# Kernel tuning notes

Hardware: AMD Instinct MI355X
Metric: run time of the kernel (lower is better)

## Reference

```python
import jax, jax.numpy as jnp
import numpy as np

N = 8192        # number of cells/nodes
D_IN = 30       # input feature dim
P_DIM = 3       # position dim
HID = 32        # attention hidden dim
D_OUT = 30      # backbone output dim
FF = 128        # MLP hidden width
SIGMA = 0.3     # spatial decay sigma


def setup_inputs() -> dict:
    key = jax.random.key(0)
    ks = jax.random.split(key, 12)
    w = lambda k, shape: (jax.random.normal(k, shape, jnp.float32) * 0.1)
    return {
        "t": jax.random.uniform(ks[0], (1,), jnp.float32),
        "Z": jax.random.normal(ks[1], (N, D_IN + P_DIM + 1), jnp.float32),
        # SpatialAttentionLayer params (Q/K/V projections + output proj)
        "Wq": w(ks[2], (D_IN, HID)), "bq": jnp.zeros((HID,), jnp.float32),
        "Wk": w(ks[3], (D_IN, HID)), "bk": jnp.zeros((HID,), jnp.float32),
        "Wv": w(ks[4], (D_IN, HID)), "bv": jnp.zeros((HID,), jnp.float32),
        "Wo": w(ks[5], (HID, D_OUT)), "bo": jnp.zeros((D_OUT,), jnp.float32),
        # LayerNorm
        "ln_g": jnp.ones((D_OUT,), jnp.float32), "ln_b": jnp.zeros((D_OUT,), jnp.float32),
        # backbone MLP: Linear(30,128) -> SiLU -> Linear(128,30)
        "W1": w(ks[6], (D_OUT, FF)), "b1": jnp.zeros((FF,), jnp.float32),
        "W2": w(ks[7], (FF, D_OUT)), "b2": jnp.zeros((D_OUT,), jnp.float32),
        # expr_head: Linear(30,30)
        "We": w(ks[8], (D_OUT, D_OUT)), "be": jnp.zeros((D_OUT,), jnp.float32),
    }


def reference(t, Z, Wq, bq, Wk, bk, Wv, bv, Wo, bo, ln_g, ln_b, W1, b1, W2, b2, We, be):
    # Z: (N, D_IN + P_DIM + 1); last column is kinetic energy (unused in fwd)
    X = Z[:, :-1]                       # (N, 33)
    P = X[:, -P_DIM:]                   # (N, 3) positions
    F = X[:, :D_IN]                     # (N, 30) features

    # --- SpatialAttentionLayer: sigma distance-decay attention, no softmax ---
    Q = F @ Wq + bq
    K = F @ Wk + bk
    V = F @ Wv + bv
    scores = (Q @ K.T) / jnp.sqrt(jnp.float32(HID))          # (N, N)
    pn = jnp.sum(P * P, axis=1)
    d2 = jnp.maximum(pn[:, None] + pn[None, :] - 2.0 * (P @ P.T), 0.0)
    decay = jnp.exp(-d2 / (2.0 * SIGMA * SIGMA))              # spatial decay kernel
    A = jax.nn.sigmoid(scores) * decay                        # no-softmax attention
    A = A / (jnp.sum(A, axis=1, keepdims=True) + 1e-8)        # row-normalized message passing
    H = (A @ V) @ Wo + bo                                     # (N, D_OUT)

    # --- LayerNorm(output_dim) ---
    mu = jnp.mean(H, axis=-1, keepdims=True)
    var = jnp.mean((H - mu) ** 2, axis=-1, keepdims=True)
    Hn = (H - mu) * jax.lax.rsqrt(var + 1e-5) * ln_g + ln_b

    # --- Linear(30,128) -> SiLU -> Linear(128,30) ---
    H2 = jax.nn.silu(Hn @ W1 + b1) @ W2 + b2

    # --- expr_head ---
    feature_velo = H2 @ We + be                               # (N, 30)

    # static_pos=True -> zero position velocities (velocity_head bypassed)
    pos_velo = jnp.zeros_like(P)                              # (N, 3)

    # kinetic energy term
    ke = 0.5 * jnp.mean(feature_velo ** 2, axis=1) + 0.5 * jnp.mean(pos_velo ** 2, axis=1)
    return jnp.concatenate([feature_velo, pos_velo, ke[:, None]], axis=1)  # (N, 34)
```

## Files before the change

### kernel.cpp

```cpp
#include <hip/hip_runtime.h>
#include <hip/hip_bf16.h>

#define N      8192
#define D_IN   30
#define HID    32
#define D_OUT  30
#define FFD    128
#define ZC     34
#define JGC    16

typedef __attribute__((ext_vector_type(8))) short short8;
typedef __attribute__((ext_vector_type(16))) float f32x16;

static __device__ __forceinline__ ushort f2bf(float x) {
    uint32_t u = __float_as_uint(x);
    uint32_t r = (u + 0x7fffu + ((u >> 16) & 1u)) >> 16;
    return (ushort)r;
}
static __device__ __forceinline__ float bf2f(ushort u) {
    return __uint_as_float(((uint32_t)u) << 16);
}
static __device__ __forceinline__ float rdlane(float v, int l) {
    return __uint_as_float(__builtin_amdgcn_readlane(__float_as_uint(v), l));
}

__global__ __launch_bounds__(256) void dv_qkv_kernel(
    const float* __restrict__ Z,
    const float* __restrict__ Wq, const float* __restrict__ bq,
    const float* __restrict__ Wk, const float* __restrict__ bk,
    const float* __restrict__ Wv, const float* __restrict__ bv,
    const float* __restrict__ Wo,
    const float* __restrict__ W2, const float* __restrict__ We,
    const float* __restrict__ b2, const float* __restrict__ be,
    ushort* __restrict__ Qb, ushort* __restrict__ Kb,
    ushort* __restrict__ VWot, ushort* __restrict__ KA,
    ushort* __restrict__ QB, float* __restrict__ W2e, float* __restrict__ b2e)
{
    __shared__ ushort sv[8][33];
    const int t = blockIdx.x * 256 + threadIdx.x;
    const int i = t >> 5;
    const int h = t & 31;
    const float* z = Z + (size_t)i * ZC;

    float q = bq[h], k = bk[h], v = bv[h];
#pragma unroll
    for (int d = 0; d < D_IN; ++d) {
        float zf = z[d];
        q = fmaf(zf, Wq[d * HID + h], q);
        k = fmaf(zf, Wk[d * HID + h], k);
        v = fmaf(zf, Wv[d * HID + h], v);
    }
    const float QS = 0.17677669529663687f * 1.4426950408889634f;
    Qb[(size_t)i * HID + h] = f2bf(q * QS);
    Kb[(size_t)i * HID + h] = f2bf(k);
    sv[threadIdx.x >> 5][h] = f2bf(v);

    if (h == 0) {
        float p0 = z[D_IN], p1 = z[D_IN + 1], p2 = z[D_IN + 2];
        const float C2 = 1.4426950408889634f / 0.18f;
        const float SC = sqrtf(2.0f * C2);
        float px = p0 * SC, py = p1 * SC, pz = p2 * SC;
        float w  = -C2 * (p0 * p0 + p1 * p1 + p2 * p2);
        ushort phx = f2bf(px), phy = f2bf(py), phz = f2bf(pz);
        ushort plx = f2bf(px - bf2f(phx));
        ushort ply = f2bf(py - bf2f(phy));
        ushort plz = f2bf(pz - bf2f(phz));
        ushort wh  = f2bf(w);
        ushort wl  = f2bf(w - bf2f(wh));
        ushort nhx = phx ^ 0x8000, nhy = phy ^ 0x8000, nhz = phz ^ 0x8000;
        ushort nlx = plx ^ 0x8000, nly = ply ^ 0x8000, nlz = plz ^ 0x8000;
        ushort nwh = wh ^ 0x8000,  nwl = wl ^ 0x8000;
        const ushort one = 0x3F80, none = 0xBF80;
        ushort ka0[8] = {nwh, nwl, none, none, nhx, nhy, nhz, nhx};
        ushort ka1[8] = {nhy, nhz, nlx, nly, nlz, nlx, nly, nlz};
        ushort qb0[8] = {one, one, wh, wl, phx, phy, phz, plx};
        ushort qb1[8] = {ply, plz, phx, phy, phz, plx, ply, plz};
        *(uint4*)&KA[(size_t)i * 8]       = *(uint4*)ka0;
        *(uint4*)&KA[((size_t)N + i) * 8] = *(uint4*)ka1;
        *(uint4*)&QB[(size_t)i * 8]       = *(uint4*)qb0;
        *(uint4*)&QB[((size_t)N + i) * 8] = *(uint4*)qb1;
    }

    if (blockIdx.x < 15) {
        int idx = blockIdx.x * 256 + threadIdx.x;
        int f = idx / 30, o = idx - f * 30;
        float acc = 0.f;
#pragma unroll
        for (int d = 0; d < D_OUT; ++d)
            acc = fmaf(W2[f * D_OUT + d], We[d * D_OUT + o], acc);
        W2e[idx] = acc;
        if (idx < D_OUT) {
            float a2 = be[idx];
#pragma unroll
            for (int d = 0; d < D_OUT; ++d)
                a2 = fmaf(b2[d], We[d * D_OUT + idx], a2);
            b2e[idx] = a2;
        }
    }

    __syncthreads();
    const int io = threadIdx.x >> 5, c = threadIdx.x & 31;
    const int ii = blockIdx.x * 8 + io;
    float val;
    if (c < 30) {
        float acc = 0.f;
#pragma unroll
        for (int hh = 0; hh < HID; ++hh)
            acc = fmaf(bf2f(sv[io][hh]), Wo[hh * D_OUT + c], acc);
        val = acc;
    } else {
        val = (c == 31) ? 1.0f : 0.f;
    }
    VWot[(size_t)c * N + ii] = f2bf(val);
}

__global__ __launch_bounds__(256, 2) void dv_attn_kernel(
    const ushort* __restrict__ Qb, const ushort* __restrict__ Kb,
    const ushort* __restrict__ VWot, const ushort* __restrict__ KA,
    const ushort* __restrict__ QB, float* __restrict__ partial, int nch)
{
    __shared__ ushort lK[128 * 32];
    __shared__ ushort lV[32 * 128];
    __shared__ ushort lKA[2][128 * 8];

    const int tid  = threadIdx.x;
    const int lane = tid & 63;
    const int wv   = tid >> 6;
    const int h2   = lane >> 5;
    const int l31  = lane & 31;
    const int rb   = blockIdx.x & 63;
    const int jg   = blockIdx.x >> 6;
    const int i0w  = rb * 128 + wv * 32;

    const ushort* qp = Qb + (size_t)(i0w + l31) * HID + h2 * 8;
    const short8 qf0 = *(const short8*)qp;
    const short8 qf1 = *(const short8*)(qp + 16);
    const short8 qaug = *(const short8*)&QB[((size_t)h2 * N + i0w + l31) * 8];

    f32x16 zacc, oacc;
#pragma unroll
    for (int r = 0; r < 16; ++r) { zacc[r] = 0.f; oacc[r] = 0.f; }

    const int cA0 = (h2 + (l31 >> 1)) & 3;
    const int cA1 = (cA0 + 2) & 3;

    const int kjr0 = tid >> 2,          kcc0 = tid & 3;
    const int kjr1 = (tid + 256) >> 2,  kcc1 = (tid + 256) & 3;
    const int kc20 = (kcc0 + (kjr0 >> 1)) & 3;
    const int kc21 = (kcc1 + (kjr1 >> 1)) & 3;
    const int vhh[4] = { tid >> 5, (tid + 256) >> 5, (tid + 512) >> 5, (tid + 768) >> 5 };
    const int vcx = tid & 31;
    const int ahalf = tid >> 7, ajj = tid & 127;

    uint4 kreg[2];
    uint2 vreg[4];
    uint4 kareg;

    {
        const int j0 = (jg * nch) << 7;
        kreg[0] = *(const uint4*)&Kb[(size_t)(j0 + kjr0) * HID + kcc0 * 8];
        kreg[1] = *(const uint4*)&Kb[(size_t)(j0 + kjr1) * HID + kcc1 * 8];
#pragma unroll
        for (int r2 = 0; r2 < 4; ++r2)
            vreg[r2] = *(const uint2*)&VWot[(size_t)vhh[r2] * N + j0 + vcx * 4];
        kareg = *(const uint4*)&KA[((size_t)ahalf * N + j0 + ajj) * 8];
    }

    for (int ch = 0; ch < nch; ++ch) {
        __syncthreads();
        *(uint4*)&lK[kjr0 * 32 + kc20 * 8] = kreg[0];
        *(uint4*)&lK[kjr1 * 32 + kc21 * 8] = kreg[1];
#pragma unroll
        for (int r2 = 0; r2 < 4; ++r2)
            *(uint2*)&lV[vhh[r2] * 128 + (vcx ^ vhh[r2]) * 4] = vreg[r2];
        *(uint4*)&lKA[ahalf][ajj * 8] = kareg;
        __syncthreads();

        if (ch + 1 < nch) {
            const int j1 = (jg * nch + ch + 1) << 7;
            kreg[0] = *(const uint4*)&Kb[(size_t)(j1 + kjr0) * HID + kcc0 * 8];
            kreg[1] = *(const uint4*)&Kb[(size_t)(j1 + kjr1) * HID + kcc1 * 8];
#pragma unroll
            for (int r2 = 0; r2 < 4; ++r2)
                vreg[r2] = *(const uint2*)&VWot[(size_t)vhh[r2] * N + j1 + vcx * 4];
            kareg = *(const uint4*)&KA[((size_t)ahalf * N + j1 + ajj) * 8];
        }

#pragma unroll
        for (int t32 = 0; t32 < 4; ++t32) {
            const ushort* krow = &lK[(t32 * 32 + l31) * 32];
            short8 kf0 = *(const short8*)&krow[cA0 * 8];
            short8 kf1 = *(const short8*)&krow[cA1 * 8];
            f32x16 s = __builtin_amdgcn_mfma_f32_32x32x16_bf16(kf0, qf0, zacc, 0, 0, 0);
            s = __builtin_amdgcn_mfma_f32_32x32x16_bf16(kf1, qf1, s, 0, 0, 0);

            short8 kaug = *(const short8*)&lKA[h2][(t32 * 32 + l31) * 8];
            f32x16 gA = __builtin_amdgcn_mfma_f32_32x32x16_bf16(kaug, qaug, zacc, 0, 0, 0);

            uint32_t pk[8];
#pragma unroll
            for (int p = 0; p < 8; ++p) {
                float eg0 = __builtin_amdgcn_exp2f(-gA[2 * p]);
                float es0 = __builtin_amdgcn_exp2f(-s[2 * p]);
                float a0  = eg0 * __builtin_amdgcn_rcpf(1.0f + es0);
                float eg1 = __builtin_amdgcn_exp2f(-gA[2 * p + 1]);
                float es1 = __builtin_amdgcn_exp2f(-s[2 * p + 1]);
                float a1  = eg1 * __builtin_amdgcn_rcpf(1.0f + es1);
                asm("v_cvt_pk_bf16_f32 %0, %1, %2" : "=v"(pk[p]) : "v"(a0), "v"(a1));
            }
            union BV { uint32_t u[4]; short8 v; };
            BV fa, fb;
            fa.u[0] = pk[0]; fa.u[1] = pk[1]; fa.u[2] = pk[2]; fa.u[3] = pk[3];
            fb.u[0] = pk[4]; fb.u[1] = pk[5]; fb.u[2] = pk[6]; fb.u[3] = pk[7];

            const ushort* vrow = &lV[l31 * 128];
            const int cb = t32 * 8 + h2;
            BV b0, b1;
            *(uint2*)&b0.u[0] = *(const uint2*)&vrow[((cb    ) ^ l31) * 4];
            *(uint2*)&b0.u[2] = *(const uint2*)&vrow[((cb + 2) ^ l31) * 4];
            *(uint2*)&b1.u[0] = *(const uint2*)&vrow[((cb + 4) ^ l31) * 4];
            *(uint2*)&b1.u[2] = *(const uint2*)&vrow[((cb + 6) ^ l31) * 4];

            oacc = __builtin_amdgcn_mfma_f32_32x32x16_bf16(fa.v, b0.v, oacc, 0, 0, 0);
            oacc = __builtin_amdgcn_mfma_f32_32x32x16_bf16(fb.v, b1.v, oacc, 0, 0, 0);
        }
    }

#pragma unroll
    for (int r = 0; r < 16; ++r) {
        int ir = (r & 3) + 8 * (r >> 2) + 4 * h2 + i0w;
        partial[(size_t)ir * (JGC * 32) + jg * 32 + l31] = oacc[r];
    }
}

__global__ __launch_bounds__(256) void dv_epilogue_kernel(
    const float* __restrict__ partial,
    const float* __restrict__ bo,
    const float* __restrict__ ln_g, const float* __restrict__ ln_b,
    const float* __restrict__ W1, const float* __restrict__ b1,
    const float* __restrict__ W2e, const float* __restrict__ b2e,
    float* __restrict__ out)
{
    __shared__ float shf[4][FFD];

    const int tid  = threadIdx.x;
    const int wv   = tid >> 6;
    const int lane = tid & 63;
    const int row  = blockIdx.x * 4 + wv;
    const int c    = lane & 31;
    const bool a30 = c < 30;
    const int  c30 = a30 ? c : 0;

    float s8 = 0.f;
    {
        const float* pp = partial + (size_t)row * (JGC * 32) + lane;
#pragma unroll
        for (int q = 0; q < 8; ++q) s8 += pp[q * 64];
    }
    float sv = s8 + __shfl_xor(s8, 32, 64);

    float rsum = __shfl(sv, 31, 32);
    float inv  = __builtin_amdgcn_rcpf(rsum + 1e-8f);
    float Hl   = a30 ? fmaf(sv, inv, bo[c30]) : 0.f;

    float x = Hl;
#pragma unroll
    for (int m = 1; m < 32; m <<= 1) x += __shfl_xor(x, m, 32);
    float mu = x * (1.0f / D_OUT);
    float d  = a30 ? (Hl - mu) : 0.f;
    float v2 = d * d;
#pragma unroll
    for (int m = 1; m < 32; m <<= 1) v2 += __shfl_xor(v2, m, 32);
    float rs = rsqrtf(v2 * (1.0f / D_OUT) + 1e-5f);
    float Hn = fmaf(d * rs, ln_g[c30], ln_b[c30]);

    float acc0 = b1[lane], acc1 = b1[lane + 64];
#pragma unroll
    for (int o = 0; o < D_OUT; ++o) {
        float ho = rdlane(Hn, o);
        acc0 = fmaf(ho, W1[o * FFD + lane], acc0);
        acc1 = fmaf(ho, W1[o * FFD + lane + 64], acc1);
    }
    const float L2E = 1.4426950408889634f;
    shf[wv][lane] =
        acc0 * __builtin_amdgcn_rcpf(1.0f + __builtin_amdgcn_exp2f(-acc0 * L2E));
    shf[wv][lane + 64] =
        acc1 * __builtin_amdgcn_rcpf(1.0f + __builtin_amdgcn_exp2f(-acc1 * L2E));

    const int half = lane >> 5;
    float acc = 0.f;
    {
        const float* hbase = &shf[wv][half * 64];
#pragma unroll
        for (int k = 0; k < 16; ++k) {
            float4 hv = *(const float4*)&hbase[k * 4];
            const int f0 = half * 64 + k * 4;
            acc = fmaf(hv.x, W2e[(f0    ) * D_OUT + c30], acc);
            acc = fmaf(hv.y, W2e[(f0 + 1) * D_OUT + c30], acc);
            acc = fmaf(hv.z, W2e[(f0 + 2) * D_OUT + c30], acc);
            acc = fmaf(hv.w, W2e[(f0 + 3) * D_OUT + c30], acc);
        }
    }
    float val = acc + __shfl_xor(acc, 32, 64) + b2e[c30];

    if (lane < 32 && a30)
        out[(size_t)row * ZC + c] = val;

    float kep = a30 ? val * val : 0.f;
#pragma unroll
    for (int m = 1; m < 32; m <<= 1) kep += __shfl_xor(kep, m, 32);
    if (lane == 0) {
        float* op = out + (size_t)row * ZC;
        op[30] = 0.f; op[31] = 0.f; op[32] = 0.f;
        op[33] = kep * (0.5f / D_OUT);
    }
}

extern "C" void kernel_launch(void* const* d_in, const int* in_sizes, int n_in,
                              void* d_out, int out_size, void* d_ws, size_t ws_size,
                              hipStream_t stream)
{
    const float* Z  = (const float*)d_in[1];
    const float* Wq = (const float*)d_in[2];
    const float* bq = (const float*)d_in[3];
    const float* Wk = (const float*)d_in[4];
    const float* bk = (const float*)d_in[5];
    const float* Wv = (const float*)d_in[6];
    const float* bv = (const float*)d_in[7];
    const float* Wo = (const float*)d_in[8];
    const float* bo = (const float*)d_in[9];
    const float* lg = (const float*)d_in[10];
    const float* lb = (const float*)d_in[11];
    const float* W1 = (const float*)d_in[12];
    const float* b1 = (const float*)d_in[13];
    const float* W2 = (const float*)d_in[14];
    const float* b2 = (const float*)d_in[15];
    const float* We = (const float*)d_in[16];
    const float* be = (const float*)d_in[17];
    float* out = (float*)d_out;

    ushort* Qb   = (ushort*)d_ws;
    ushort* Kb   = Qb + (size_t)N * HID;
    ushort* VWot = Kb + (size_t)N * HID;
    ushort* KA   = VWot + (size_t)N * HID;
    ushort* QB   = KA + (size_t)N * 16;
    float*  W2e  = (float*)(QB + (size_t)N * 16);
    float*  b2e  = W2e + FFD * D_OUT;
    float*  partial = b2e + 32;

    int nch = N / (JGC * 128);

    hipLaunchKernelGGL(dv_qkv_kernel, dim3((N * HID) / 256), dim3(256), 0, stream,
                       Z, Wq, bq, Wk, bk, Wv, bv, Wo, W2, We, b2, be,
                       Qb, Kb, VWot, KA, QB, W2e, b2e);
    hipLaunchKernelGGL(dv_attn_kernel, dim3(64 * JGC), dim3(256), 0, stream,
                       Qb, Kb, VWot, KA, QB, partial, nch);
    hipLaunchKernelGGL(dv_epilogue_kernel, dim3(N / 4), dim3(256), 0, stream,
                       partial, bo, lg, lb, W1, b1, W2e, b2e, out);
}
```

Baseline: 58.44 us.

## Morton-sort points and cull far key chunks via AABB distance test

Adds a spatial sort: points are binned into a 16^3 Morton grid with histogram, scan and scatter kernels. Q/K/V are built in sorted order, and an AABB kernel computes per-128-point chunk bounds. The attention kernel skips any key chunk whose box distance to the query block makes the Gaussian decay below about 2^-24. The intent is to avoid most of the N^2 attention work. In exchange it adds five extra launches plus a memset and atomics, introduces a tiny approximation error, and may unbalance work across blocks.

```diff
diff --git a/kernel.cpp b/kernel.cpp
--- a/kernel.cpp
+++ b/kernel.cpp
@@ -8,6 +8,9 @@
 #define FFD    128
 #define ZC     34
 #define JGC    16
+#define NCH    4
+#define NCHUNK 64
+#define DCUT2  48.0f
 
 typedef __attribute__((ext_vector_type(8))) short short8;
 typedef __attribute__((ext_vector_type(16))) float f32x16;
@@ -24,8 +27,57 @@
     return __uint_as_float(__builtin_amdgcn_readlane(__float_as_uint(v), l));
 }
 
+__global__ __launch_bounds__(256) void dv_hist_kernel(
+    const float* __restrict__ Z, int* __restrict__ key, int* __restrict__ hist)
+{
+    const int i = blockIdx.x * 256 + threadIdx.x;
+    const float* z = Z + (size_t)i * ZC;
+    float x = z[D_IN], y = z[D_IN + 1], w = z[D_IN + 2];
+    int qx = (int)((x + 3.f) * (16.f / 6.f)); qx = qx < 0 ? 0 : (qx > 15 ? 15 : qx);
+    int qy = (int)((y + 3.f) * (16.f / 6.f)); qy = qy < 0 ? 0 : (qy > 15 ? 15 : qy);
+    int qz = (int)((w + 3.f) * (16.f / 6.f)); qz = qz < 0 ? 0 : (qz > 15 ? 15 : qz);
+    int k = 0;
+#pragma unroll
+    for (int b = 0; b < 4; ++b) {
+        k |= ((qx >> b) & 1) << (3 * b + 2);
+        k |= ((qy >> b) & 1) << (3 * b + 1);
+        k |= ((qz >> b) & 1) << (3 * b);
+    }
+    key[i] = k;
+    atomicAdd(&hist[k], 1);
+}
+
+__global__ __launch_bounds__(256) void dv_scan_kernel(
+    const int* __restrict__ hist, int* __restrict__ offs)
+{
+    __shared__ int ls[256];
+    const int t = threadIdx.x;
+    int loc[16], s = 0;
+#pragma unroll
+    for (int k = 0; k < 16; ++k) { loc[k] = hist[t * 16 + k]; s += loc[k]; }
+    ls[t] = s;
+    __syncthreads();
+    for (int d = 1; d < 256; d <<= 1) {
+        int v = (t >= d) ? ls[t - d] : 0;
+        __syncthreads();
+        ls[t] += v;
+        __syncthreads();
+    }
+    int excl = ls[t] - s;
+#pragma unroll
+    for (int k = 0; k < 16; ++k) { offs[t * 16 + k] = excl; excl += loc[k]; }
+}
+
+__global__ __launch_bounds__(256) void dv_scatter_kernel(
+    const int* __restrict__ key, int* __restrict__ offs, int* __restrict__ perm)
+{
+    const int i = blockIdx.x * 256 + threadIdx.x;
+    int dst = atomicAdd(&offs[key[i]], 1);
+    perm[dst] = i;
+}
+
 __global__ __launch_bounds__(256) void dv_qkv_kernel(
-    const float* __restrict__ Z,
+    const float* __restrict__ Z, const int* __restrict__ perm,
     const float* __restrict__ Wq, const float* __restrict__ bq,
     const float* __restrict__ Wk, const float* __restrict__ bk,
     const float* __restrict__ Wv, const float* __restrict__ bv,
@@ -34,13 +86,15 @@
     const float* __restrict__ b2, const float* __restrict__ be,
     ushort* __restrict__ Qb, ushort* __restrict__ Kb,
     ushort* __restrict__ VWot, ushort* __restrict__ KA,
-    ushort* __restrict__ QB, float* __restrict__ W2e, float* __restrict__ b2e)
+    ushort* __restrict__ QB, float4* __restrict__ pos_s,
+    float* __restrict__ W2e, float* __restrict__ b2e)
 {
     __shared__ ushort sv[8][33];
     const int t = blockIdx.x * 256 + threadIdx.x;
     const int i = t >> 5;
     const int h = t & 31;
-    const float* z = Z + (size_t)i * ZC;
+    const int orig = perm[i];
+    const float* z = Z + (size_t)orig * ZC;
 
     float q = bq[h], k = bk[h], v = bv[h];
 #pragma unroll
@@ -61,6 +115,7 @@
         const float SC = sqrtf(2.0f * C2);
         float px = p0 * SC, py = p1 * SC, pz = p2 * SC;
         float w  = -C2 * (p0 * p0 + p1 * p1 + p2 * p2);
+        pos_s[i] = make_float4(px, py, pz, 0.f);
         ushort phx = f2bf(px), phy = f2bf(py), phz = f2bf(pz);
         ushort plx = f2bf(px - bf2f(phx));
         ushort ply = f2bf(py - bf2f(phy));
@@ -114,10 +169,41 @@
     VWot[(size_t)c * N + ii] = f2bf(val);
 }
 
+__global__ __launch_bounds__(128) void dv_aabb_kernel(
+    const float4* __restrict__ pos_s, float4* __restrict__ aabb)
+{
+    const int cid = blockIdx.x, t = threadIdx.x;
+    float4 p = pos_s[cid * 128 + t];
+    float mnx = p.x, mny = p.y, mnz = p.z;
+    float mxx = p.x, mxy = p.y, mxz = p.z;
+#pragma unroll
+    for (int m = 1; m < 64; m <<= 1) {
+        mnx = fminf(mnx, __shfl_xor(mnx, m, 64));
+        mny = fminf(mny, __shfl_xor(mny, m, 64));
+        mnz = fminf(mnz, __shfl_xor(mnz, m, 64));
+        mxx = fmaxf(mxx, __shfl_xor(mxx, m, 64));
+        mxy = fmaxf(mxy, __shfl_xor(mxy, m, 64));
+        mxz = fmaxf(mxz, __shfl_xor(mxz, m, 64));
+    }
+    __shared__ float4 smn[2], smx[2];
+    if ((t & 63) == 0) {
+        smn[t >> 6] = make_float4(mnx, mny, mnz, 0.f);
+        smx[t >> 6] = make_float4(mxx, mxy, mxz, 0.f);
+    }
+    __syncthreads();
+    if (t == 0) {
+        float4 a = smn[0], b = smn[1];
+        aabb[cid * 2] = make_float4(fminf(a.x, b.x), fminf(a.y, b.y), fminf(a.z, b.z), 0.f);
+        a = smx[0]; b = smx[1];
+        aabb[cid * 2 + 1] = make_float4(fmaxf(a.x, b.x), fmaxf(a.y, b.y), fmaxf(a.z, b.z), 0.f);
+    }
+}
+
 __global__ __launch_bounds__(256, 2) void dv_attn_kernel(
     const ushort* __restrict__ Qb, const ushort* __restrict__ Kb,
     const ushort* __restrict__ VWot, const ushort* __restrict__ KA,
-    const ushort* __restrict__ QB, float* __restrict__ partial, int nch)
+    const ushort* __restrict__ QB, const float4* __restrict__ aabb,
+    float* __restrict__ partial)
 {
     __shared__ ushort lK[128 * 32];
     __shared__ ushort lV[32 * 128];
@@ -144,6 +230,21 @@
     const int cA0 = (h2 + (l31 >> 1)) & 3;
     const int cA1 = (cA0 + 2) & 3;
 
+    uint32_t mask = 0;
+    {
+        float4 amin = aabb[2 * rb], amax = aabb[2 * rb + 1];
+#pragma unroll
+        for (int c = 0; c < NCH; ++c) {
+            int cid = jg * NCH + c;
+            float4 bmin = aabb[2 * cid], bmax = aabb[2 * cid + 1];
+            float dx = fmaxf(0.f, fmaxf(amin.x - bmax.x, bmin.x - amax.x));
+            float dy = fmaxf(0.f, fmaxf(amin.y - bmax.y, bmin.y - amax.y));
+            float dz = fmaxf(0.f, fmaxf(amin.z - bmax.z, bmin.z - amax.z));
+            float d2 = fmaf(dx, dx, fmaf(dy, dy, dz * dz));
+            if (d2 > DCUT2) mask |= (1u << c);
+        }
+    }
+
     const int kjr0 = tid >> 2,          kcc0 = tid & 3;
     const int kjr1 = (tid + 256) >> 2,  kcc1 = (tid + 256) & 3;
     const int kc20 = (kcc0 + (kjr0 >> 1)) & 3;
@@ -156,17 +257,26 @@
     uint2 vreg[4];
     uint4 kareg;
 
-    {
-        const int j0 = (jg * nch) << 7;
+    auto LOADC = [&](int c) {
+        const int j0 = (jg * NCH + c) << 7;
         kreg[0] = *(const uint4*)&Kb[(size_t)(j0 + kjr0) * HID + kcc0 * 8];
         kreg[1] = *(const uint4*)&Kb[(size_t)(j0 + kjr1) * HID + kcc1 * 8];
 #pragma unroll
         for (int r2 = 0; r2 < 4; ++r2)
             vreg[r2] = *(const uint2*)&VWot[(size_t)vhh[r2] * N + j0 + vcx * 4];
         kareg = *(const uint4*)&KA[((size_t)ahalf * N + j0 + ajj) * 8];
-    }
-
-    for (int ch = 0; ch < nch; ++ch) {
+    };
+
+    int cur = -1;
+    for (int c = 0; c < NCH; ++c)
+        if (!(mask & (1u << c))) { cur = c; break; }
+    if (cur >= 0) LOADC(cur);
+
+    while (cur >= 0) {
+        int nxt = -1;
+        for (int c = cur + 1; c < NCH; ++c)
+            if (!(mask & (1u << c))) { nxt = c; break; }
+
         __syncthreads();
         *(uint4*)&lK[kjr0 * 32 + kc20 * 8] = kreg[0];
         *(uint4*)&lK[kjr1 * 32 + kc21 * 8] = kreg[1];
@@ -176,15 +286,7 @@
         *(uint4*)&lKA[ahalf][ajj * 8] = kareg;
         __syncthreads();
 
-        if (ch + 1 < nch) {
-            const int j1 = (jg * nch + ch + 1) << 7;
-            kreg[0] = *(const uint4*)&Kb[(size_t)(j1 + kjr0) * HID + kcc0 * 8];
-            kreg[1] = *(const uint4*)&Kb[(size_t)(j1 + kjr1) * HID + kcc1 * 8];
-#pragma unroll
-            for (int r2 = 0; r2 < 4; ++r2)
-                vreg[r2] = *(const uint2*)&VWot[(size_t)vhh[r2] * N + j1 + vcx * 4];
-            kareg = *(const uint4*)&KA[((size_t)ahalf * N + j1 + ajj) * 8];
-        }
+        if (nxt >= 0) LOADC(nxt);
 
 #pragma unroll
         for (int t32 = 0; t32 < 4; ++t32) {
@@ -224,6 +326,7 @@
             oacc = __builtin_amdgcn_mfma_f32_32x32x16_bf16(fa.v, b0.v, oacc, 0, 0, 0);
             oacc = __builtin_amdgcn_mfma_f32_32x32x16_bf16(fb.v, b1.v, oacc, 0, 0, 0);
         }
+        cur = nxt;
     }
 
 #pragma unroll
@@ -234,7 +337,7 @@
 }
 
 __global__ __launch_bounds__(256) void dv_epilogue_kernel(
-    const float* __restrict__ partial,
+    const float* __restrict__ partial, const int* __restrict__ perm,
     const float* __restrict__ bo,
     const float* __restrict__ ln_g, const float* __restrict__ ln_b,
     const float* __restrict__ W1, const float* __restrict__ b1,
@@ -247,6 +350,7 @@
     const int wv   = tid >> 6;
     const int lane = tid & 63;
     const int row  = blockIdx.x * 4 + wv;
+    const int orow = perm[row];
     const int c    = lane & 31;
     const bool a30 = c < 30;
     const int  c30 = a30 ? c : 0;
@@ -304,13 +408,13 @@
     float val = acc + __shfl_xor(acc, 32, 64) + b2e[c30];
 
     if (lane < 32 && a30)
-        out[(size_t)row * ZC + c] = val;
+        out[(size_t)orow * ZC + c] = val;
 
     float kep = a30 ? val * val : 0.f;
 #pragma unroll
     for (int m = 1; m < 32; m <<= 1) kep += __shfl_xor(kep, m, 32);
     if (lane == 0) {
-        float* op = out + (size_t)row * ZC;
+        float* op = out + (size_t)orow * ZC;
         op[30] = 0.f; op[31] = 0.f; op[32] = 0.f;
         op[33] = kep * (0.5f / D_OUT);
     }
@@ -346,15 +450,28 @@
     ushort* QB   = KA + (size_t)N * 16;
     float*  W2e  = (float*)(QB + (size_t)N * 16);
     float*  b2e  = W2e + FFD * D_OUT;
-    float*  partial = b2e + 32;
-
-    int nch = N / (JGC * 128);
-
+    float4* pos_s = (float4*)(b2e + 32);
+    float4* aabb  = pos_s + N;
+    int*    key   = (int*)(aabb + 2 * NCHUNK);
+    int*    perm  = key + N;
+    int*    hist  = perm + N;
+    int*    offs  = hist + 4096;
+    float*  partial = (float*)(offs + 4096);
+
+    hipMemsetAsync(hist, 0, 4096 * sizeof(int), stream);
+    hipLaunchKernelGGL(dv_hist_kernel, dim3(N / 256), dim3(256), 0, stream,
+                       Z, key, hist);
+    hipLaunchKernelGGL(dv_scan_kernel, dim3(1), dim3(256), 0, stream,
+                       hist, offs);
+    hipLaunchKernelGGL(dv_scatter_kernel, dim3(N / 256), dim3(256), 0, stream,
+                       key, offs, perm);
     hipLaunchKernelGGL(dv_qkv_kernel, dim3((N * HID) / 256), dim3(256), 0, stream,
-                       Z, Wq, bq, Wk, bk, Wv, bv, Wo, W2, We, b2, be,
-                       Qb, Kb, VWot, KA, QB, W2e, b2e);
+                       Z, perm, Wq, bq, Wk, bk, Wv, bv, Wo, W2, We, b2, be,
+                       Qb, Kb, VWot, KA, QB, pos_s, W2e, b2e);
+    hipLaunchKernelGGL(dv_aabb_kernel, dim3(NCHUNK), dim3(128), 0, stream,
+                       pos_s, aabb);
     hipLaunchKernelGGL(dv_attn_kernel, dim3(64 * JGC), dim3(256), 0, stream,
-                       Qb, Kb, VWot, KA, QB, partial, nch);
+                       Qb, Kb, VWot, KA, QB, aabb, partial);
     hipLaunchKernelGGL(dv_epilogue_kernel, dim3(N / 4), dim3(256), 0, stream,
-                       partial, bo, lg, lb, W1, b1, W2e, b2e, out);
-}
+                       partial, perm, bo, lg, lb, W1, b1, W2e, b2e, out);
+}
```

New measurement: 75.66 us. 1.29x slower.

## Preload whole V slice into LDS once and read K fragments directly from global

Applied to the files above, without the earlier changes.

The attention kernel no longer streams K, KA and V through shared memory chunk by chunk with register double-buffering and two barriers per chunk. It loads the block's entire 512-column V slice into LDS once behind a single barrier, and each wave then reads its K and K-augment MFMA fragments straight from global memory (L2/L1). This removes the per-chunk barriers and LDS staging of K, but adds redundant global K loads across the four waves, exposes global load latency directly before the MFMAs, and drops the two-blocks-per-CU occupancy hint. The j-range per block is now hardcoded to 512 instead of using the nch parameter.

```diff
diff --git a/kernel.cpp b/kernel.cpp
--- a/kernel.cpp
+++ b/kernel.cpp
@@ -114,14 +114,12 @@
     VWot[(size_t)c * N + ii] = f2bf(val);
 }
 
-__global__ __launch_bounds__(256, 2) void dv_attn_kernel(
+__global__ __launch_bounds__(256) void dv_attn_kernel(
     const ushort* __restrict__ Qb, const ushort* __restrict__ Kb,
     const ushort* __restrict__ VWot, const ushort* __restrict__ KA,
-    const ushort* __restrict__ QB, float* __restrict__ partial, int nch)
+    const ushort* __restrict__ QB, float* __restrict__ partial)
 {
-    __shared__ ushort lK[128 * 32];
-    __shared__ ushort lV[32 * 128];
-    __shared__ ushort lKA[2][128 * 8];
+    __shared__ ushort lV[32 * 512];
 
     const int tid  = threadIdx.x;
     const int lane = tid & 63;
@@ -131,70 +129,41 @@
     const int rb   = blockIdx.x & 63;
     const int jg   = blockIdx.x >> 6;
     const int i0w  = rb * 128 + wv * 32;
+    const int jgbase = jg << 9;
 
     const ushort* qp = Qb + (size_t)(i0w + l31) * HID + h2 * 8;
     const short8 qf0 = *(const short8*)qp;
     const short8 qf1 = *(const short8*)(qp + 16);
     const short8 qaug = *(const short8*)&QB[((size_t)h2 * N + i0w + l31) * 8];
 
+#pragma unroll
+    for (int rep = 0; rep < 16; ++rep) {
+        int idx = tid + rep * 256;
+        int hh = idx >> 7;
+        int cc = idx & 127;
+        int cs = cc ^ hh;
+        *(uint2*)&lV[hh * 512 + cs * 4] =
+            *(const uint2*)&VWot[(size_t)hh * N + jgbase + cc * 4];
+    }
+    __syncthreads();
+
     f32x16 zacc, oacc;
 #pragma unroll
     for (int r = 0; r < 16; ++r) { zacc[r] = 0.f; oacc[r] = 0.f; }
 
-    const int cA0 = (h2 + (l31 >> 1)) & 3;
-    const int cA1 = (cA0 + 2) & 3;
-
-    const int kjr0 = tid >> 2,          kcc0 = tid & 3;
-    const int kjr1 = (tid + 256) >> 2,  kcc1 = (tid + 256) & 3;
-    const int kc20 = (kcc0 + (kjr0 >> 1)) & 3;
-    const int kc21 = (kcc1 + (kjr1 >> 1)) & 3;
-    const int vhh[4] = { tid >> 5, (tid + 256) >> 5, (tid + 512) >> 5, (tid + 768) >> 5 };
-    const int vcx = tid & 31;
-    const int ahalf = tid >> 7, ajj = tid & 127;
-
-    uint4 kreg[2];
-    uint2 vreg[4];
-    uint4 kareg;
-
-    {
-        const int j0 = (jg * nch) << 7;
-        kreg[0] = *(const uint4*)&Kb[(size_t)(j0 + kjr0) * HID + kcc0 * 8];
-        kreg[1] = *(const uint4*)&Kb[(size_t)(j0 + kjr1) * HID + kcc1 * 8];
-#pragma unroll
-        for (int r2 = 0; r2 < 4; ++r2)
-            vreg[r2] = *(const uint2*)&VWot[(size_t)vhh[r2] * N + j0 + vcx * 4];
-        kareg = *(const uint4*)&KA[((size_t)ahalf * N + j0 + ajj) * 8];
-    }
-
-    for (int ch = 0; ch < nch; ++ch) {
-        __syncthreads();
-        *(uint4*)&lK[kjr0 * 32 + kc20 * 8] = kreg[0];
-        *(uint4*)&lK[kjr1 * 32 + kc21 * 8] = kreg[1];
-#pragma unroll
-        for (int r2 = 0; r2 < 4; ++r2)
-            *(uint2*)&lV[vhh[r2] * 128 + (vcx ^ vhh[r2]) * 4] = vreg[r2];
-        *(uint4*)&lKA[ahalf][ajj * 8] = kareg;
-        __syncthreads();
-
-        if (ch + 1 < nch) {
-            const int j1 = (jg * nch + ch + 1) << 7;
-            kreg[0] = *(const uint4*)&Kb[(size_t)(j1 + kjr0) * HID + kcc0 * 8];
-            kreg[1] = *(const uint4*)&Kb[(size_t)(j1 + kjr1) * HID + kcc1 * 8];
-#pragma unroll
-            for (int r2 = 0; r2 < 4; ++r2)
-                vreg[r2] = *(const uint2*)&VWot[(size_t)vhh[r2] * N + j1 + vcx * 4];
-            kareg = *(const uint4*)&KA[((size_t)ahalf * N + j1 + ajj) * 8];
-        }
-
+    const ushort* vrow = &lV[l31 * 512];
+
+    for (int ch = 0; ch < 4; ++ch) {
 #pragma unroll
         for (int t32 = 0; t32 < 4; ++t32) {
-            const ushort* krow = &lK[(t32 * 32 + l31) * 32];
-            short8 kf0 = *(const short8*)&krow[cA0 * 8];
-            short8 kf1 = *(const short8*)&krow[cA1 * 8];
+            const int j0 = jgbase + ch * 128 + t32 * 32;
+            const ushort* krow = &Kb[(size_t)(j0 + l31) * HID + h2 * 8];
+            short8 kf0 = *(const short8*)krow;
+            short8 kf1 = *(const short8*)(krow + 16);
+            short8 kaug = *(const short8*)&KA[((size_t)h2 * N + j0 + l31) * 8];
+
             f32x16 s = __builtin_amdgcn_mfma_f32_32x32x16_bf16(kf0, qf0, zacc, 0, 0, 0);
             s = __builtin_amdgcn_mfma_f32_32x32x16_bf16(kf1, qf1, s, 0, 0, 0);
-
-            short8 kaug = *(const short8*)&lKA[h2][(t32 * 32 + l31) * 8];
             f32x16 gA = __builtin_amdgcn_mfma_f32_32x32x16_bf16(kaug, qaug, zacc, 0, 0, 0);
 
             uint32_t pk[8];
@@ -213,8 +182,7 @@
             fa.u[0] = pk[0]; fa.u[1] = pk[1]; fa.u[2] = pk[2]; fa.u[3] = pk[3];
             fb.u[0] = pk[4]; fb.u[1] = pk[5]; fb.u[2] = pk[6]; fb.u[3] = pk[7];
 
-            const ushort* vrow = &lV[l31 * 128];
-            const int cb = t32 * 8 + h2;
+            const int cb = ch * 32 + t32 * 8 + h2;
             BV b0, b1;
             *(uint2*)&b0.u[0] = *(const uint2*)&vrow[((cb    ) ^ l31) * 4];
             *(uint2*)&b0.u[2] = *(const uint2*)&vrow[((cb + 2) ^ l31) * 4];
@@ -348,13 +316,11 @@
     float*  b2e  = W2e + FFD * D_OUT;
     float*  partial = b2e + 32;
 
-    int nch = N / (JGC * 128);
-
     hipLaunchKernelGGL(dv_qkv_kernel, dim3((N * HID) / 256), dim3(256), 0, stream,
                        Z, Wq, bq, Wk, bk, Wv, bv, Wo, W2, We, b2, be,
                        Qb, Kb, VWot, KA, QB, W2e, b2e);
     hipLaunchKernelGGL(dv_attn_kernel, dim3(64 * JGC), dim3(256), 0, stream,
-                       Qb, Kb, VWot, KA, QB, partial, nch);
+                       Qb, Kb, VWot, KA, QB, partial);
     hipLaunchKernelGGL(dv_epilogue_kernel, dim3(N / 4), dim3(256), 0, stream,
                        partial, bo, lg, lb, W1, b1, W2e, b2e, out);
 }
```

New measurement: 64.43 us. 10.2% more time.
